# Kernel tuning notes

Measured on AMD Instinct MI355X. Metric: run time of the kernel, lower is better.

The kernel has to match this reference:

```python
import jax, jax.numpy as jnp
import numpy as np

C = 512
H_HEADS = 8
HEAD_DIM = C // H_HEADS


def setup_inputs() -> dict:
    key = jax.random.key(0)
    ks = jax.random.split(key, 6)
    B, Hs, Ws = 16, 32, 32
    x = jax.random.normal(ks[0], (B, C, Hs, Ws), dtype=jnp.float32)
    qkv_w = jax.random.normal(ks[1], (3 * C, C), dtype=jnp.float32) * 0.02
    proj_w = jax.random.normal(ks[2], (C, C), dtype=jnp.float32) * 0.02
    proj_b = jnp.zeros((C,), dtype=jnp.float32)
    ln_g = jnp.ones((C,), dtype=jnp.float32)
    ln_b = jnp.zeros((C,), dtype=jnp.float32)
    return {"x": x, "qkv_w": qkv_w, "proj_w": proj_w, "proj_b": proj_b,
            "ln_g": ln_g, "ln_b": ln_b}


def _layernorm(x, g, b, eps=1e-5):
    mu = jnp.mean(x, axis=-1, keepdims=True)
    var = jnp.var(x, axis=-1, keepdims=True)
    return (x - mu) * jax.lax.rsqrt(var + eps) * g + b


def reference(x, qkv_w, proj_w, proj_b, ln_g, ln_b):
    B, Cc, Hs, Ws = x.shape
    N = Hs * Ws
    # (B, N, C)
    x_flat = x.reshape(B, Cc, N).transpose(0, 2, 1)
    x_norm = _layernorm(x_flat, ln_g, ln_b)
    # qkv: torch Linear y = x @ W^T
    qkv = x_norm @ qkv_w.T  # (B, N, 3C)
    qkv = qkv.reshape(B, N, 3, H_HEADS, HEAD_DIM).transpose(2, 0, 3, 1, 4)
    q, k, v = qkv[0], qkv[1], qkv[2]  # (B, h, N, d)
    scale = HEAD_DIM ** -0.5
    attn = jnp.einsum('bhnd,bhmd->bhnm', q, k) * scale
    attn = jax.nn.softmax(attn, axis=-1)
    out = jnp.einsum('bhnm,bhmd->bhnd', attn, v)  # (B, h, N, d)
    out = out.transpose(0, 2, 1, 3).reshape(B, N, Cc)
    out = out @ proj_w.T + proj_b
    out = out + x_flat
    return out.transpose(0, 2, 1).reshape(B, Cc, Hs, Ws)
```

## Files before the change

kernel.cpp:

```cpp
#include <hip/hip_runtime.h>
#include <stdint.h>

typedef unsigned short u16;
typedef __attribute__((ext_vector_type(4))) float f32x4;
typedef __attribute__((ext_vector_type(8))) short s16x8;
typedef __attribute__((ext_vector_type(4))) unsigned short u16x4;
typedef __attribute__((ext_vector_type(8))) unsigned short u16x8;
typedef __attribute__((ext_vector_type(4))) unsigned int u32x4;

__device__ __forceinline__ u16 f2bf(float f) {
  union { float f; uint32_t u; } v; v.f = f;
  uint32_t r = (v.u + 0x7FFFu + ((v.u >> 16) & 1u)) >> 16;
  return (u16)r;
}

__device__ __forceinline__ uint32_t cvtpk(float lo, float hi) {
  uint32_t r;
  asm("v_cvt_pk_bf16_f32 %0, %1, %2" : "=v"(r) : "v"(lo), "v"(hi));
  return r;
}

__device__ __forceinline__ float fexp2(float x) {
#if __has_builtin(__builtin_amdgcn_exp2f)
  return __builtin_amdgcn_exp2f(x);
#else
  float r; asm("v_exp_f32 %0, %1" : "=v"(r) : "v"(x)); return r;
#endif
}

__device__ __forceinline__ void gload_lds16(const void* g, void* l) {
  __builtin_amdgcn_global_load_lds((const __attribute__((address_space(1))) uint32_t*)g,
                                   (__attribute__((address_space(3))) uint32_t*)l, 16, 0, 0);
}

__global__ __launch_bounds__(256) void cvt_kernel(const float* __restrict__ src,
                                                  u16* __restrict__ dst, int n) {
  const int i = (blockIdx.x * 256 + threadIdx.x) * 4;
  if (i < n) {
    f32x4 v = *(const f32x4*)(src + i);
    u16x4 p;
    p[0] = f2bf(v[0]); p[1] = f2bf(v[1]); p[2] = f2bf(v[2]); p[3] = f2bf(v[3]);
    *(u16x4*)(dst + i) = p;
  }
}

__global__ __launch_bounds__(256) void ln_kernel(const float* __restrict__ x,
                                                 const float* __restrict__ lng,
                                                 const float* __restrict__ lnb,
                                                 u16* __restrict__ xn) {
  __shared__ float xt[16][516];
  __shared__ float ps[16][16], pq[16][16];
  __shared__ float smu[16], srs[16];
  const int tid = threadIdx.x;
  const int tok0 = blockIdx.x << 4;
  const int b = tok0 >> 10;
  const int nb = tok0 & 1023;
  const float* xb = x + (size_t)b * 512 * 1024 + nb;
  {
    const int n4 = (tid & 3) * 4;
    const int cr = tid >> 2;
#pragma unroll
    for (int it = 0; it < 8; ++it) {
      const int c = it * 64 + cr;
      f32x4 v = *(const f32x4*)(xb + (size_t)c * 1024 + n4);
      xt[n4 + 0][c] = v[0]; xt[n4 + 1][c] = v[1];
      xt[n4 + 2][c] = v[2]; xt[n4 + 3][c] = v[3];
    }
  }
  __syncthreads();
  {
    const int n = tid & 15, part = tid >> 4;
    float s = 0.f, q = 0.f;
#pragma unroll
    for (int i = 0; i < 8; ++i) {
      f32x4 v = *(const f32x4*)&xt[n][part * 32 + i * 4];
#pragma unroll
      for (int j = 0; j < 4; ++j) { s += v[j]; q += v[j] * v[j]; }
    }
    ps[part][n] = s; pq[part][n] = q;
  }
  __syncthreads();
  if (tid < 16) {
    float s = 0.f, q = 0.f;
#pragma unroll
    for (int p = 0; p < 16; ++p) { s += ps[p][tid]; q += pq[p][tid]; }
    const float mu = s * (1.f / 512.f);
    const float var = q * (1.f / 512.f) - mu * mu;
    smu[tid] = mu; srs[tid] = rsqrtf(var + 1e-5f);
  }
  __syncthreads();
  {
    const int n = tid >> 4, sub = tid & 15;
    const float mu = smu[n], rs = srs[n];
    u16* dst = xn + (size_t)(tok0 + n) * 512;
#pragma unroll
    for (int i = 0; i < 4; ++i) {
      const int c = (sub + 16 * i) * 8;
      f32x4 v0 = *(const f32x4*)&xt[n][c];
      f32x4 v1 = *(const f32x4*)&xt[n][c + 4];
      f32x4 g0 = *(const f32x4*)(lng + c);
      f32x4 g1 = *(const f32x4*)(lng + c + 4);
      f32x4 b0 = *(const f32x4*)(lnb + c);
      f32x4 b1 = *(const f32x4*)(lnb + c + 4);
      union { u32x4 w; u16x8 v; } pk;
      float r0 = (v0[0] - mu) * rs * g0[0] + b0[0];
      float r1 = (v0[1] - mu) * rs * g0[1] + b0[1];
      float r2 = (v0[2] - mu) * rs * g0[2] + b0[2];
      float r3 = (v0[3] - mu) * rs * g0[3] + b0[3];
      float r4 = (v1[0] - mu) * rs * g1[0] + b1[0];
      float r5 = (v1[1] - mu) * rs * g1[1] + b1[1];
      float r6 = (v1[2] - mu) * rs * g1[2] + b1[2];
      float r7 = (v1[3] - mu) * rs * g1[3] + b1[3];
      pk.w[0] = cvtpk(r0, r1); pk.w[1] = cvtpk(r2, r3);
      pk.w[2] = cvtpk(r4, r5); pk.w[3] = cvtpk(r6, r7);
      *(u16x8*)(dst + c) = pk.v;
    }
  }
}

template <int EPI>
__global__ __launch_bounds__(256) void gemm_bt(const u16* __restrict__ A,
                                               const u16* __restrict__ Bw,
                                               void* __restrict__ Cout,
                                               u16* __restrict__ vt,
                                               const float* __restrict__ bias,
                                               const float* __restrict__ resid,
                                               int M, int N, int K,
                                               long bsz, long csz, long rsz) {
  __shared__ union {
    struct { u16 A[3][128 * 32]; u16 B[3][128 * 32]; } m;
    u16 t[128 * 136];
  } sg;
  const int tid = threadIdx.x;
  const int w = tid >> 6, lane = tid & 63;
  const int lg = lane >> 4, l15 = lane & 15;
  const int wr = w >> 1, wc = w & 1;
  int m0, n0, z;
  if (EPI == 0) {
    const int blk = blockIdx.x;
    const int c = blk & 7, j = blk >> 3;
    m0 = (c * 16 + j / 12) * 128;
    n0 = (j % 12) * 128;
    z = 0;
  } else {
    const int blk = blockIdx.x;
    const int c = blk & 7, j = blk >> 3;
    z = c * 2 + (j >> 5);
    const int mn = j & 31;
    m0 = (mn >> 3) * 128;
    n0 = (mn & 7) * 128;
  }
  const u16* Bz = Bw + (size_t)z * bsz;
  const float* Rz = (EPI == 1) ? resid + (size_t)z * rsz : nullptr;

  f32x4 acc[4][4];
#pragma unroll
  for (int i = 0; i < 4; ++i)
#pragma unroll
    for (int j = 0; j < 4; ++j) acc[i][j] = (f32x4){0.f, 0.f, 0.f, 0.f};

  const int sr = lane >> 2, sch = (lane & 3) * 8;
  const u16* ap = A + (size_t)(m0 + w * 32 + sr) * K + sch;
  const u16* bp = Bz + (size_t)(n0 + w * 32 + sr) * K + sch;

  auto stage = [&](int buf) {
    gload_lds16(ap,          &sg.m.A[buf][(w * 32 + 0) * 32]);
    gload_lds16(ap + 16 * K, &sg.m.A[buf][(w * 32 + 16) * 32]);
    gload_lds16(bp,          &sg.m.B[buf][(w * 32 + 0) * 32]);
    gload_lds16(bp + 16 * K, &sg.m.B[buf][(w * 32 + 16) * 32]);
    ap += 32; bp += 32;
  };
  auto compute = [&](int buf) {
    s16x8 af[4], bfr[4];
#pragma unroll
    for (int mi = 0; mi < 4; ++mi)
      af[mi] = *(const s16x8*)&sg.m.A[buf][(wr * 64 + mi * 16 + l15) * 32 + lg * 8];
#pragma unroll
    for (int ni = 0; ni < 4; ++ni)
      bfr[ni] = *(const s16x8*)&sg.m.B[buf][(wc * 64 + ni * 16 + l15) * 32 + lg * 8];
#pragma unroll
    for (int mi = 0; mi < 4; ++mi)
#pragma unroll
      for (int ni = 0; ni < 4; ++ni)
        acc[mi][ni] = __builtin_amdgcn_mfma_f32_16x16x32_bf16(af[mi], bfr[ni], acc[mi][ni], 0, 0, 0);
  };

  stage(0); stage(1); stage(2);
#define GSTEP(BUF, NCNT, DOSTAGE)                                  \
  asm volatile("s_waitcnt vmcnt(" #NCNT ")" ::: "memory");         \
  __builtin_amdgcn_s_barrier();                                    \
  asm volatile("" ::: "memory");                                   \
  compute(BUF);                                                    \
  asm volatile("" ::: "memory");                                   \
  __builtin_amdgcn_s_barrier();                                    \
  if (DOSTAGE) stage(BUF);
#pragma unroll 1
  for (int it = 0; it < 4; ++it) {
    GSTEP(0, 8, 1)
    GSTEP(1, 8, 1)
    GSTEP(2, 8, 1)
  }
  GSTEP(0, 8, 1)
  GSTEP(1, 8, 0)
  GSTEP(2, 4, 0)
  asm volatile("s_waitcnt vmcnt(0)" ::: "memory");
  __builtin_amdgcn_s_barrier();
  asm volatile("" ::: "memory");
  compute(0);
#undef GSTEP

  if (EPI == 0) {
    u16* C = (u16*)Cout;
    if (n0 < 1024) {
      const float ce = (n0 < 512) ? 0.125f * 1.44269504f : 1.0f;
      __syncthreads();
#pragma unroll
      for (int mi = 0; mi < 4; ++mi)
#pragma unroll
        for (int ni = 0; ni < 4; ++ni) {
          const int colb = wc * 64 + ni * 16 + l15;
#pragma unroll
          for (int r = 0; r < 4; ++r) {
            const int rowb = wr * 64 + mi * 16 + lg * 4 + r;
            sg.t[rowb * 136 + colb] = (u16)cvtpk(acc[mi][ni][r] * ce, 0.f);
          }
        }
      __syncthreads();
#pragma unroll
      for (int itr = 0; itr < 8; ++itr) {
        const int rowb = itr * 16 + (tid >> 4);
        u16x8 v8 = *(const u16x8*)&sg.t[rowb * 136 + (tid & 15) * 8];
        *(u16x8*)(C + (size_t)(m0 + rowb) * 1024 + n0 + (tid & 15) * 8) = v8;
      }
    } else {
#pragma unroll
      for (int mi = 0; mi < 4; ++mi)
#pragma unroll
        for (int ni = 0; ni < 4; ++ni) {
          const int vcol = n0 - 1024 + wc * 64 + ni * 16 + l15;
          const int hh = vcol >> 6, d = vcol & 63;
          const int token = m0 + wr * 64 + mi * 16 + lg * 4;
          const int b = token >> 10, g15 = (token >> 6) & 15;
          const int p = 32 * (mi >> 1) + 8 * lg + 4 * (mi & 1);
          union { uint32_t w[2]; u16x4 v; } pk;
          pk.w[0] = cvtpk(acc[mi][ni][0], acc[mi][ni][1]);
          pk.w[1] = cvtpk(acc[mi][ni][2], acc[mi][ni][3]);
          *(u16x4*)&vt[(size_t)((b * 8 + hh) * 64 + d) * 1024 + g15 * 64 + p] = pk.v;
        }
    }
  } else {
    float* C = (float*)Cout + (size_t)z * csz;
#pragma unroll
    for (int mi = 0; mi < 4; ++mi)
#pragma unroll
      for (int ni = 0; ni < 4; ++ni) {
        const int col = n0 + wc * 64 + ni * 16 + l15;
#pragma unroll
        for (int r = 0; r < 4; ++r) {
          const int row = m0 + wr * 64 + mi * 16 + lg * 4 + r;
          C[(size_t)row * N + col] = acc[mi][ni][r] + bias[row] + Rz[(size_t)row * N + col];
        }
      }
  }
}

__global__ __launch_bounds__(256, 4) void attn_kernel(const u16* __restrict__ qk,
                                                      const u16* __restrict__ vt,
                                                      u16* __restrict__ ao) {
  __shared__ union {
    struct { u16 K[2][64 * 64]; u16 V[2][64 * 64]; } s;
    struct { float O[4][16][68]; float ls[4 * 32]; } e;
  } sm;
  const int tid = threadIdx.x;
  const int w = tid >> 6, lane = tid & 63;
  const int lg = lane >> 4, l15 = lane & 15;
  const int blk = blockIdx.x;
  const int qb = (blk >> 3) & 7;
  const int bh = (blk & 7) | ((blk >> 6) << 3);
  const int b = bh >> 3, h = bh & 7;
  const size_t qbase = (size_t)b * 1024 * 1024;
  const size_t vbase = (size_t)bh * 64 * 1024;
  const int qtok0 = qb * 128 + w * 32;

  s16x8 qf[2][2];
#pragma unroll
  for (int s = 0; s < 2; ++s)
#pragma unroll
    for (int qg = 0; qg < 2; ++qg)
      qf[s][qg] = *(const s16x8*)(qk + qbase + (size_t)(qtok0 + qg * 16 + l15) * 1024 +
                                  h * 64 + lg * 8 + 32 * s);

  f32x4 o[2][4];
  f32x4 lacc[2];
#pragma unroll
  for (int qg = 0; qg < 2; ++qg) {
    lacc[qg] = (f32x4){0.f, 0.f, 0.f, 0.f};
#pragma unroll
    for (int db = 0; db < 4; ++db) o[qg][db] = (f32x4){0.f, 0.f, 0.f, 0.f};
  }
  s16x8 ones;
#pragma unroll
  for (int j = 0; j < 8; ++j) ones[j] = (short)0x3F80;

  const int srr = lane >> 3, sch = lane & 7;
  const int row0 = w * 16 + srr, row1 = row0 + 8;
  const u16* kp0 = qk + qbase + (size_t)row0 * 1024 + 512 + h * 64 + ((sch ^ (row0 & 7)) * 8);
  const u16* kp1 = qk + qbase + (size_t)row1 * 1024 + 512 + h * 64 + ((sch ^ (row1 & 7)) * 8);
  const u16* vp0 = vt + vbase + (size_t)row0 * 1024 + ((sch ^ (row0 & 7)) * 8);
  const u16* vp1 = vt + vbase + (size_t)row1 * 1024 + ((sch ^ (row1 & 7)) * 8);

  auto stage = [&](int buf) {
    gload_lds16(kp0, &sm.s.K[buf][(w * 16 + 0) * 64]);
    gload_lds16(kp1, &sm.s.K[buf][(w * 16 + 8) * 64]);
    gload_lds16(vp0, &sm.s.V[buf][(w * 16 + 0) * 64]);
    gload_lds16(vp1, &sm.s.V[buf][(w * 16 + 8) * 64]);
    kp0 += 64 * 1024; kp1 += 64 * 1024;
    vp0 += 64; vp1 += 64;
  };

  auto compute = [&](int buf) {
    f32x4 st[4][2];
#pragma unroll
    for (int kg = 0; kg < 4; ++kg)
#pragma unroll
      for (int qg = 0; qg < 2; ++qg) st[kg][qg] = (f32x4){0.f, 0.f, 0.f, 0.f};
    __builtin_amdgcn_s_setprio(1);
#pragma unroll
    for (int s = 0; s < 2; ++s)
#pragma unroll
      for (int kg = 0; kg < 4; ++kg) {
        const int row = kg * 16 + l15;
        s16x8 kf = *(const s16x8*)&sm.s.K[buf][row * 64 +
                                              ((lg * 8 + 32 * s) ^ ((row & 7) << 3))];
#pragma unroll
        for (int qg = 0; qg < 2; ++qg)
          st[kg][qg] = __builtin_amdgcn_mfma_f32_16x16x32_bf16(kf, qf[s][qg], st[kg][qg], 0, 0, 0);
      }
    __builtin_amdgcn_s_setprio(0);

    s16x8 pa[2][2];
#pragma unroll
    for (int qg = 0; qg < 2; ++qg) {
      float pv[16];
#pragma unroll
      for (int kg = 0; kg < 4; ++kg)
#pragma unroll
        for (int r = 0; r < 4; ++r)
          pv[kg * 4 + r] = fexp2(st[kg][qg][r]);
#pragma unroll
      for (int kh = 0; kh < 2; ++kh) {
        union { u32x4 wd; s16x8 v; } pk;
        pk.wd[0] = cvtpk(pv[8 * kh + 0], pv[8 * kh + 1]);
        pk.wd[1] = cvtpk(pv[8 * kh + 2], pv[8 * kh + 3]);
        pk.wd[2] = cvtpk(pv[8 * kh + 4], pv[8 * kh + 5]);
        pk.wd[3] = cvtpk(pv[8 * kh + 6], pv[8 * kh + 7]);
        pa[qg][kh] = pk.v;
      }
    }

    __builtin_amdgcn_s_setprio(1);
#pragma unroll
    for (int kh = 0; kh < 2; ++kh) {
#pragma unroll
      for (int db = 0; db < 4; ++db) {
        const int d = db * 16 + l15;
        s16x8 vf = *(const s16x8*)&sm.s.V[buf][d * 64 +
                                               ((kh * 32 + lg * 8) ^ ((d & 7) << 3))];
#pragma unroll
        for (int qg = 0; qg < 2; ++qg)
          o[qg][db] = __builtin_amdgcn_mfma_f32_16x16x32_bf16(pa[qg][kh], vf, o[qg][db], 0, 0, 0);
      }
#pragma unroll
      for (int qg = 0; qg < 2; ++qg)
        lacc[qg] = __builtin_amdgcn_mfma_f32_16x16x32_bf16(pa[qg][kh], ones, lacc[qg], 0, 0, 0);
    }
    __builtin_amdgcn_s_setprio(0);
  };

  stage(0);
#pragma unroll 1
  for (int it = 0; it < 7; ++it) {
    stage(1);
    asm volatile("s_waitcnt vmcnt(4)" ::: "memory");
    __builtin_amdgcn_s_barrier();
    asm volatile("" ::: "memory");
    compute(0);
    asm volatile("" ::: "memory");
    __builtin_amdgcn_s_barrier();
    stage(0);
    asm volatile("s_waitcnt vmcnt(4)" ::: "memory");
    __builtin_amdgcn_s_barrier();
    asm volatile("" ::: "memory");
    compute(1);
    asm volatile("" ::: "memory");
    __builtin_amdgcn_s_barrier();
  }
  stage(1);
  asm volatile("s_waitcnt vmcnt(4)" ::: "memory");
  __builtin_amdgcn_s_barrier();
  asm volatile("" ::: "memory");
  compute(0);
  asm volatile("" ::: "memory");
  __builtin_amdgcn_s_barrier();
  asm volatile("s_waitcnt vmcnt(0)" ::: "memory");
  __builtin_amdgcn_s_barrier();
  asm volatile("" ::: "memory");
  compute(1);

  __syncthreads();
  if (l15 == 0) {
#pragma unroll
    for (int qg = 0; qg < 2; ++qg)
#pragma unroll
      for (int r = 0; r < 4; ++r)
        sm.e.ls[w * 32 + qg * 16 + lg * 4 + r] = lacc[qg][r];
  }
#pragma unroll
  for (int half = 0; half < 2; ++half) {
#pragma unroll
    for (int db = 0; db < 4; ++db)
#pragma unroll
      for (int r = 0; r < 4; ++r)
        sm.e.O[w][lg * 4 + r][db * 16 + l15] = o[half][db][r];
    __syncthreads();
    {
      const int q = lane & 15, dh = lane >> 4;
      const float inv = 1.0f / sm.e.ls[w * 32 + half * 16 + q];
      u16* dst = ao + (size_t)(b * 1024 + qtok0 + half * 16 + q) * 512 + h * 64 + dh * 16;
      f32x4 v0 = *(const f32x4*)&sm.e.O[w][q][dh * 16 + 0];
      f32x4 v1 = *(const f32x4*)&sm.e.O[w][q][dh * 16 + 4];
      f32x4 v2 = *(const f32x4*)&sm.e.O[w][q][dh * 16 + 8];
      f32x4 v3 = *(const f32x4*)&sm.e.O[w][q][dh * 16 + 12];
      union { u32x4 wd; u16x8 v; } p0, p1;
      p0.wd[0] = cvtpk(v0[0] * inv, v0[1] * inv);
      p0.wd[1] = cvtpk(v0[2] * inv, v0[3] * inv);
      p0.wd[2] = cvtpk(v1[0] * inv, v1[1] * inv);
      p0.wd[3] = cvtpk(v1[2] * inv, v1[3] * inv);
      p1.wd[0] = cvtpk(v2[0] * inv, v2[1] * inv);
      p1.wd[1] = cvtpk(v2[2] * inv, v2[3] * inv);
      p1.wd[2] = cvtpk(v3[0] * inv, v3[1] * inv);
      p1.wd[3] = cvtpk(v3[2] * inv, v3[3] * inv);
      *(u16x8*)(dst + 0) = p0.v;
      *(u16x8*)(dst + 8) = p1.v;
    }
    __syncthreads();
  }
}

extern "C" void kernel_launch(void* const* d_in, const int* in_sizes, int n_in,
                              void* d_out, int out_size, void* d_ws, size_t ws_size,
                              hipStream_t stream) {
  const float* x      = (const float*)d_in[0];
  const float* qkv_w  = (const float*)d_in[1];
  const float* proj_w = (const float*)d_in[2];
  const float* proj_b = (const float*)d_in[3];
  const float* ln_g   = (const float*)d_in[4];
  const float* ln_b   = (const float*)d_in[5];
  float* out = (float*)d_out;

  char* ws = (char*)d_ws;
  u16* xn  = (u16*)ws;
  u16* qk  = (u16*)(ws + (size_t)16 * 1024 * 1024);
  u16* vt  = (u16*)(ws + (size_t)48 * 1024 * 1024);
  u16* ao  = (u16*)(ws + (size_t)64 * 1024 * 1024);
  u16* qw  = (u16*)(ws + (size_t)80 * 1024 * 1024);
  u16* pw  = qw + 1536 * 512;

  cvt_kernel<<<768, 256, 0, stream>>>(qkv_w, qw, 1536 * 512);
  cvt_kernel<<<256, 256, 0, stream>>>(proj_w, pw, 512 * 512);
  ln_kernel<<<1024, 256, 0, stream>>>(x, ln_g, ln_b, xn);
  gemm_bt<0><<<1536, 256, 0, stream>>>(xn, qw, qk, vt, nullptr, nullptr,
                                       16384, 1024, 512, 0, 0, 0);
  attn_kernel<<<1024, 256, 0, stream>>>(qk, vt, ao);
  gemm_bt<1><<<512, 256, 0, stream>>>(pw, ao, out, nullptr, proj_b, x,
                                      512, 1024, 512,
                                      (long)1024 * 512, (long)512 * 1024,
                                      (long)512 * 1024);
}
```

Measured before the change: 218.7 us.

## Stage proj epilogue through LDS for vectorized stores; split attention launch in two

The output-projection epilogue now writes accumulators to shared memory in two half-tile passes, then reads rows back as float4 to add bias and residual and store coalesced 16-byte writes. This replaces the scattered scalar global loads and stores of the old epilogue. The attention kernel takes a query-block offset and is launched twice with half the grid each, changing block-to-work mapping. The cost is extra LDS traffic and barriers in the epilogue, plus a second attention kernel launch.

Result: slower. 310.4 us (+41.9%).

```diff
diff --git a/kernel.cpp b/kernel.cpp
--- a/kernel.cpp
+++ b/kernel.cpp
@@ -130,6 +130,7 @@
   __shared__ union {
     struct { u16 A[3][128 * 32]; u16 B[3][128 * 32]; } m;
     u16 t[128 * 136];
+    float tf[64][132];
   } sg;
   const int tid = threadIdx.x;
   const int w = tid >> 6, lane = tid & 63;
@@ -251,22 +252,40 @@
   } else {
     float* C = (float*)Cout + (size_t)z * csz;
 #pragma unroll
-    for (int mi = 0; mi < 4; ++mi)
-#pragma unroll
-      for (int ni = 0; ni < 4; ++ni) {
-        const int col = n0 + wc * 64 + ni * 16 + l15;
-#pragma unroll
-        for (int r = 0; r < 4; ++r) {
-          const int row = m0 + wr * 64 + mi * 16 + lg * 4 + r;
-          C[(size_t)row * N + col] = acc[mi][ni][r] + bias[row] + Rz[(size_t)row * N + col];
-        }
-      }
+    for (int p = 0; p < 2; ++p) {
+      __syncthreads();
+      if (wr == p) {
+#pragma unroll
+        for (int mi = 0; mi < 4; ++mi)
+#pragma unroll
+          for (int ni = 0; ni < 4; ++ni) {
+            const int colb = wc * 64 + ni * 16 + l15;
+#pragma unroll
+            for (int r = 0; r < 4; ++r)
+              sg.tf[mi * 16 + lg * 4 + r][colb] = acc[mi][ni][r];
+          }
+      }
+      __syncthreads();
+#pragma unroll
+      for (int jj = 0; jj < 8; ++jj) {
+        const int rl = jj * 8 + (tid >> 5);
+        const int colb = (tid & 31) * 4;
+        const int row = m0 + p * 64 + rl;
+        f32x4 v = *(const f32x4*)&sg.tf[rl][colb];
+        const float bv = bias[row];
+        f32x4 rz = *(const f32x4*)(Rz + (size_t)row * N + n0 + colb);
+        v[0] += bv + rz[0]; v[1] += bv + rz[1];
+        v[2] += bv + rz[2]; v[3] += bv + rz[3];
+        *(f32x4*)(C + (size_t)row * N + n0 + colb) = v;
+      }
+    }
   }
 }
 
 __global__ __launch_bounds__(256, 4) void attn_kernel(const u16* __restrict__ qk,
                                                       const u16* __restrict__ vt,
-                                                      u16* __restrict__ ao) {
+                                                      u16* __restrict__ ao,
+                                                      int qoff) {
   __shared__ union {
     struct { u16 K[2][64 * 64]; u16 V[2][64 * 64]; } s;
     struct { float O[4][16][68]; float ls[4 * 32]; } e;
@@ -275,8 +294,8 @@
   const int w = tid >> 6, lane = tid & 63;
   const int lg = lane >> 4, l15 = lane & 15;
   const int blk = blockIdx.x;
-  const int qb = (blk >> 3) & 7;
-  const int bh = (blk & 7) | ((blk >> 6) << 3);
+  const int qb = ((blk >> 3) & 3) + qoff;
+  const int bh = (blk & 7) | ((blk >> 5) << 3);
   const int b = bh >> 3, h = bh & 7;
   const size_t qbase = (size_t)b * 1024 * 1024;
   const size_t vbase = (size_t)bh * 64 * 1024;
@@ -471,7 +490,8 @@
   ln_kernel<<<1024, 256, 0, stream>>>(x, ln_g, ln_b, xn);
   gemm_bt<0><<<1536, 256, 0, stream>>>(xn, qw, qk, vt, nullptr, nullptr,
                                        16384, 1024, 512, 0, 0, 0);
-  attn_kernel<<<1024, 256, 0, stream>>>(qk, vt, ao);
+  attn_kernel<<<512, 256, 0, stream>>>(qk, vt, ao, 0);
+  attn_kernel<<<512, 256, 0, stream>>>(qk, vt, ao, 4);
   gemm_bt<1><<<512, 256, 0, stream>>>(pw, ao, out, nullptr, proj_b, x,
                                       512, 1024, 512,
                                       (long)1024 * 512, (long)512 * 1024,
```
